# Performance work log

Measured on AMD Instinct MI355X. Metric: run time of the kernel, lower is better.

Reference implementation:

```python
import jax, jax.numpy as jnp
import numpy as np

LUMINANCE_Q = np.array([
    [16, 11, 10, 16, 24, 40, 51, 61],
    [12, 12, 14, 19, 26, 58, 60, 55],
    [14, 13, 16, 24, 40, 57, 69, 56],
    [14, 17, 22, 29, 51, 87, 80, 62],
    [18, 22, 37, 56, 68, 109, 103, 77],
    [24, 36, 55, 64, 81, 104, 113, 92],
    [49, 64, 78, 87, 103, 121, 120, 101],
    [72, 92, 95, 98, 112, 100, 103, 99]], dtype=np.float64) / 100.0

def _dct_matrix():
    # C[k, n] = grid_factors[k] * cos(pi*k*(2n+1)/16); grid_factors = 2*[1/sqrt(32), 1/sqrt(16)x7]
    k = np.arange(8)[:, None]
    n = np.arange(8)[None, :]
    a = np.full(8, 2.0 / np.sqrt(2 * 8))
    a[0] = 2.0 / np.sqrt(4 * 8)
    C = a[:, None] * np.cos(np.pi * k * (2 * n + 1) / 16.0)
    return jnp.asarray(C, dtype=jnp.float32)

DCT_C = _dct_matrix()
Q_TABLE = jnp.asarray(LUMINANCE_Q, dtype=jnp.float32)

def setup_inputs() -> dict:
    key = jax.random.key(0)
    k1, k2 = jax.random.split(key)
    B, H, W = 16, 1024, 1024
    # pixel-like values around 128
    image = 128.0 + 40.0 * jax.random.normal(k1, (B, 1, H, W), dtype=jnp.float32)
    quality_factor = jax.random.randint(k2, (B,), 1, 100).astype(jnp.float32)
    return {"image": image, "quality_factor": quality_factor}

def reference(image, quality_factor):
    B, _, H, W = image.shape
    # Set_QF: factor per batch element, shape [B,1,1,1,1]
    factor = jnp.where(quality_factor < 50.0,
                       5000.0 / quality_factor,
                       200.0 - 2.0 * quality_factor).reshape(B, 1, 1, 1, 1)
    # Image_2_Blocks: [B, H/8, 8, W/8, 8] -> [B, 8, 8, H/8, W/8], then center
    blocks = image.reshape(B, H // 8, 8, W // 8, 8).transpose(0, 2, 4, 1, 3) - 128.0
    # 2D orthonormal DCT-II over the two 8-wide in-block axes (axes 1 then 2)
    dct = jnp.einsum('un,vm,bnmij->buvij', DCT_C, DCT_C, blocks)
    out = dct / (factor * Q_TABLE[None, :, :, None, None])
    # quantize=False: no rounding
    return out.reshape(B, 64, H // 8, W // 8)
```

## Files before the change

kernel.cpp:

```cpp
#include <hip/hip_runtime.h>
#include <cstddef>


static constexpr float COSTAB[32] = {
     0.50000000000000000f,  0.49039264020161522f,  0.46193976625564337f,
     0.41573480615127262f,  0.35355339059327373f,  0.27778511650980114f,
     0.19134171618254492f,  0.09754516100806417f,  0.00000000000000000f,
    -0.09754516100806417f, -0.19134171618254492f, -0.27778511650980114f,
    -0.35355339059327373f, -0.41573480615127262f, -0.46193976625564337f,
    -0.49039264020161522f, -0.50000000000000000f, -0.49039264020161522f,
    -0.46193976625564337f, -0.41573480615127262f, -0.35355339059327373f,
    -0.27778511650980114f, -0.19134171618254492f, -0.09754516100806417f,
     0.00000000000000000f,  0.09754516100806417f,  0.19134171618254492f,
     0.27778511650980114f,  0.35355339059327373f,  0.41573480615127262f,
     0.46193976625564337f,  0.49039264020161522f,
};

__device__ __host__ __forceinline__ constexpr float dctC(int k, int n) {
    return (k == 0) ? 0.35355339059327373f
                    : COSTAB[(k * (2 * n + 1)) & 31];
}

static constexpr float LUMQ[64] = {
    16, 11, 10, 16, 24, 40, 51, 61,
    12, 12, 14, 19, 26, 58, 60, 55,
    14, 13, 16, 24, 40, 57, 69, 56,
    14, 17, 22, 29, 51, 87, 80, 62,
    18, 22, 37, 56, 68, 109, 103, 77,
    24, 36, 55, 64, 81, 104, 113, 92,
    49, 64, 78, 87, 103, 121, 120, 101,
    72, 92, 95, 98, 112, 100, 103, 99,
};

__device__ __host__ __forceinline__ constexpr float invQ(int u, int v) {
    return 100.0f / LUMQ[u * 8 + v];
}

__global__ __launch_bounds__(256) void jpeg_dct_quant_kernel(
    const float* __restrict__ img,
    const float* __restrict__ qfv,
    float* __restrict__ out)
{
    const int bid = blockIdx.x * 256 + threadIdx.x;
    const int j = bid & 127;
    const int i = (bid >> 7) & 127;
    const int b = bid >> 14;

    const float* src = img + ((size_t)b << 20) + (size_t)(i * 8) * 1024 + j * 8;

    float D[8][8];
    #pragma unroll
    for (int u = 0; u < 8; ++u)
        #pragma unroll
        for (int v = 0; v < 8; ++v)
            D[u][v] = 0.0f;

    #pragma unroll
    for (int n = 0; n < 8; ++n) {
        const float4 r0 = *reinterpret_cast<const float4*>(src + (size_t)n * 1024);
        const float4 r1 = *reinterpret_cast<const float4*>(src + (size_t)n * 1024 + 4);
        const float x[8] = {
            r0.x - 128.0f, r0.y - 128.0f, r0.z - 128.0f, r0.w - 128.0f,
            r1.x - 128.0f, r1.y - 128.0f, r1.z - 128.0f, r1.w - 128.0f,
        };

        float y[8];
        #pragma unroll
        for (int v = 0; v < 8; ++v) {
            float acc = 0.0f;
            #pragma unroll
            for (int m = 0; m < 8; ++m)
                acc += x[m] * dctC(v, m);
            y[v] = acc;
        }

        #pragma unroll
        for (int u = 0; u < 8; ++u) {
            const float cu = dctC(u, n);
            #pragma unroll
            for (int v = 0; v < 8; ++v)
                D[u][v] += cu * y[v];
        }
    }

    const float qf = qfv[b];
    const float factor = (qf < 50.0f) ? (5000.0f / qf) : (200.0f - 2.0f * qf);
    const float invf = 1.0f / factor;

    float* dst = out + ((size_t)b << 20) + (size_t)i * 128 + j;
    #pragma unroll
    for (int u = 0; u < 8; ++u)
        #pragma unroll
        for (int v = 0; v < 8; ++v)
            dst[(size_t)(u * 8 + v) * 16384] = D[u][v] * (invf * invQ(u, v));
}

extern "C" void kernel_launch(void* const* d_in, const int* in_sizes, int n_in,
                              void* d_out, int out_size, void* d_ws, size_t ws_size,
                              hipStream_t stream) {
    const float* img = (const float*)d_in[0];
    const float* qfv = (const float*)d_in[1];
    float* out = (float*)d_out;

    jpeg_dct_quant_kernel<<<1024, 256, 0, stream>>>(img, qfv, out);
}
```

Measured before the change: 111.3 us.

## Split DCT output rows across two threads, use even/odd butterfly, nontemporal stores

Each 8x8 block is now handled by two threads that each compute four of the eight output frequency rows, doubling the grid to 2048 blocks and halving the accumulator registers per thread. The row DCT uses an even/odd butterfly to halve multiplies, and the -128 centering is folded into a single DC correction of -1024. Output writes become nontemporal stores, and launch bounds request higher occupancy. The cost is that both threads of a pair load and transform the same input rows, so the row-pass work is duplicated.

```diff
diff --git a/kernel.cpp b/kernel.cpp
--- a/kernel.cpp
+++ b/kernel.cpp
@@ -36,52 +36,57 @@
     return 100.0f / LUMQ[u * 8 + v];
 }
 
-__global__ __launch_bounds__(256) void jpeg_dct_quant_kernel(
+__global__ __launch_bounds__(256, 6) void jpeg_dct_quant_kernel(
     const float* __restrict__ img,
     const float* __restrict__ qfv,
     float* __restrict__ out)
 {
-    const int bid = blockIdx.x * 256 + threadIdx.x;
-    const int j = bid & 127;
-    const int i = (bid >> 7) & 127;
-    const int b = bid >> 14;
+    const int tid  = threadIdx.x;
+    const int half = tid >> 7;
+    const int j    = tid & 127;
+    const int row  = blockIdx.x;
+    const int b    = row >> 7;
+    const int i    = row & 127;
+    const int u0   = half * 4;
 
     const float* src = img + ((size_t)b << 20) + (size_t)(i * 8) * 1024 + j * 8;
 
-    float D[8][8];
+    float acc[4][8];
     #pragma unroll
-    for (int u = 0; u < 8; ++u)
+    for (int uu = 0; uu < 4; ++uu)
         #pragma unroll
         for (int v = 0; v < 8; ++v)
-            D[u][v] = 0.0f;
+            acc[uu][v] = 0.0f;
 
     #pragma unroll
     for (int n = 0; n < 8; ++n) {
         const float4 r0 = *reinterpret_cast<const float4*>(src + (size_t)n * 1024);
         const float4 r1 = *reinterpret_cast<const float4*>(src + (size_t)n * 1024 + 4);
-        const float x[8] = {
-            r0.x - 128.0f, r0.y - 128.0f, r0.z - 128.0f, r0.w - 128.0f,
-            r1.x - 128.0f, r1.y - 128.0f, r1.z - 128.0f, r1.w - 128.0f,
-        };
+        const float s0 = r0.x + r1.w, s1 = r0.y + r1.z;
+        const float s2 = r0.z + r1.y, s3 = r0.w + r1.x;
+        const float d0 = r0.x - r1.w, d1 = r0.y - r1.z;
+        const float d2 = r0.z - r1.y, d3 = r0.w - r1.x;
 
         float y[8];
         #pragma unroll
-        for (int v = 0; v < 8; ++v) {
-            float acc = 0.0f;
-            #pragma unroll
-            for (int m = 0; m < 8; ++m)
-                acc += x[m] * dctC(v, m);
-            y[v] = acc;
-        }
+        for (int v = 0; v < 8; v += 2)
+            y[v] = s0 * dctC(v, 0) + s1 * dctC(v, 1)
+                 + s2 * dctC(v, 2) + s3 * dctC(v, 3);
+        #pragma unroll
+        for (int v = 1; v < 8; v += 2)
+            y[v] = d0 * dctC(v, 0) + d1 * dctC(v, 1)
+                 + d2 * dctC(v, 2) + d3 * dctC(v, 3);
 
         #pragma unroll
-        for (int u = 0; u < 8; ++u) {
-            const float cu = dctC(u, n);
+        for (int uu = 0; uu < 4; ++uu) {
+            const float cu = dctC(u0 + uu, n);
             #pragma unroll
             for (int v = 0; v < 8; ++v)
-                D[u][v] += cu * y[v];
+                acc[uu][v] += cu * y[v];
         }
     }
+
+    if (half == 0) acc[0][0] -= 1024.0f;
 
     const float qf = qfv[b];
     const float factor = (qf < 50.0f) ? (5000.0f / qf) : (200.0f - 2.0f * qf);
@@ -89,10 +94,14 @@
 
     float* dst = out + ((size_t)b << 20) + (size_t)i * 128 + j;
     #pragma unroll
-    for (int u = 0; u < 8; ++u)
+    for (int uu = 0; uu < 4; ++uu) {
+        const int u = u0 + uu;
         #pragma unroll
-        for (int v = 0; v < 8; ++v)
-            dst[(size_t)(u * 8 + v) * 16384] = D[u][v] * (invf * invQ(u, v));
+        for (int v = 0; v < 8; ++v) {
+            const float val = acc[uu][v] * (invf * invQ(u, v));
+            __builtin_nontemporal_store(val, dst + (size_t)(u * 8 + v) * 16384);
+        }
+    }
 }
 
 extern "C" void kernel_launch(void* const* d_in, const int* in_sizes, int n_in,
@@ -102,5 +111,5 @@
     const float* qfv = (const float*)d_in[1];
     float* out = (float*)d_out;
 
-    jpeg_dct_quant_kernel<<<1024, 256, 0, stream>>>(img, qfv, out);
+    jpeg_dct_quant_kernel<<<2048, 256, 0, stream>>>(img, qfv, out);
 }
```

Measured after the change: 186.5 us. +67.6%, slower.

## Replace matrix-multiply DCT with AAN fast butterfly DCT and folded scaling

Applied to the files above, without the earlier changes.

Replaces the dense separable 8x8 DCT matrix products with the Arai-Agui-Nakajima butterfly factorization applied to rows and then columns. The AAN output scale factors are folded into the per-coefficient quantization multiplier. The 128 centering is dropped from every pixel and applied once as a DC correction. This cuts per-block floating-point work substantially, but the kernel is likely bound by memory traffic, and the DC-offset trick changes rounding slightly.

```diff
diff --git a/kernel.cpp b/kernel.cpp
--- a/kernel.cpp
+++ b/kernel.cpp
@@ -2,26 +2,7 @@
 #include <cstddef>
 
 
-static constexpr float COSTAB[32] = {
-     0.50000000000000000f,  0.49039264020161522f,  0.46193976625564337f,
-     0.41573480615127262f,  0.35355339059327373f,  0.27778511650980114f,
-     0.19134171618254492f,  0.09754516100806417f,  0.00000000000000000f,
-    -0.09754516100806417f, -0.19134171618254492f, -0.27778511650980114f,
-    -0.35355339059327373f, -0.41573480615127262f, -0.46193976625564337f,
-    -0.49039264020161522f, -0.50000000000000000f, -0.49039264020161522f,
-    -0.46193976625564337f, -0.41573480615127262f, -0.35355339059327373f,
-    -0.27778511650980114f, -0.19134171618254492f, -0.09754516100806417f,
-     0.00000000000000000f,  0.09754516100806417f,  0.19134171618254492f,
-     0.27778511650980114f,  0.35355339059327373f,  0.41573480615127262f,
-     0.46193976625564337f,  0.49039264020161522f,
-};
-
-__device__ __host__ __forceinline__ constexpr float dctC(int k, int n) {
-    return (k == 0) ? 0.35355339059327373f
-                    : COSTAB[(k * (2 * n + 1)) & 31];
-}
-
-static constexpr float LUMQ[64] = {
+static constexpr double LUMQ[64] = {
     16, 11, 10, 16, 24, 40, 51, 61,
     12, 12, 14, 19, 26, 58, 60, 55,
     14, 13, 16, 24, 40, 57, 69, 56,
@@ -32,8 +13,46 @@
     72, 92, 95, 98, 112, 100, 103, 99,
 };
 
-__device__ __host__ __forceinline__ constexpr float invQ(int u, int v) {
-    return 100.0f / LUMQ[u * 8 + v];
+static constexpr double AANS[8] = {
+    1.0, 1.3870398453221475, 1.3065629648763766, 1.1758756024193588,
+    1.0, 0.7856949583871022, 0.5411961001461970, 0.2758993792829430,
+};
+
+__device__ __host__ __forceinline__ constexpr float outScale(int u, int v) {
+    return (float)(100.0 / (LUMQ[u * 8 + v] * 8.0 * AANS[u] * AANS[v]));
+}
+
+__device__ __forceinline__ void aan_dct8(float& x0, float& x1, float& x2,
+                                         float& x3, float& x4, float& x5,
+                                         float& x6, float& x7) {
+    const float t0 = x0 + x7, t7 = x0 - x7;
+    const float t1 = x1 + x6, t6 = x1 - x6;
+    const float t2 = x2 + x5, t5 = x2 - x5;
+    const float t3 = x3 + x4, t4 = x3 - x4;
+
+    float t10 = t0 + t3;
+    const float t13 = t0 - t3;
+    const float t11 = t1 + t2;
+    const float t12 = t1 - t2;
+    x0 = t10 + t11;
+    x4 = t10 - t11;
+    const float z1 = (t12 + t13) * 0.70710678118654752f;
+    x2 = t13 + z1;
+    x6 = t13 - z1;
+
+    t10 = t4 + t5;
+    const float u11 = t5 + t6;
+    const float u12 = t6 + t7;
+    const float z5 = (t10 - u12) * 0.38268343236508977f;
+    const float z2 = 0.54119610014619698f * t10 + z5;
+    const float z4 = 1.30656296487637653f * u12 + z5;
+    const float z3 = u11 * 0.70710678118654752f;
+    const float z11 = t7 + z3;
+    const float z13 = t7 - z3;
+    x5 = z13 + z2;
+    x3 = z13 - z2;
+    x1 = z11 + z4;
+    x7 = z11 - z4;
 }
 
 __global__ __launch_bounds__(256) void jpeg_dct_quant_kernel(
@@ -48,40 +67,26 @@
 
     const float* src = img + ((size_t)b << 20) + (size_t)(i * 8) * 1024 + j * 8;
 
-    float D[8][8];
-    #pragma unroll
-    for (int u = 0; u < 8; ++u)
-        #pragma unroll
-        for (int v = 0; v < 8; ++v)
-            D[u][v] = 0.0f;
-
+    float m[8][8];
     #pragma unroll
     for (int n = 0; n < 8; ++n) {
         const float4 r0 = *reinterpret_cast<const float4*>(src + (size_t)n * 1024);
         const float4 r1 = *reinterpret_cast<const float4*>(src + (size_t)n * 1024 + 4);
-        const float x[8] = {
-            r0.x - 128.0f, r0.y - 128.0f, r0.z - 128.0f, r0.w - 128.0f,
-            r1.x - 128.0f, r1.y - 128.0f, r1.z - 128.0f, r1.w - 128.0f,
-        };
+        m[n][0] = r0.x; m[n][1] = r0.y; m[n][2] = r0.z; m[n][3] = r0.w;
+        m[n][4] = r1.x; m[n][5] = r1.y; m[n][6] = r1.z; m[n][7] = r1.w;
+    }
 
-        float y[8];
-        #pragma unroll
-        for (int v = 0; v < 8; ++v) {
-            float acc = 0.0f;
-            #pragma unroll
-            for (int m = 0; m < 8; ++m)
-                acc += x[m] * dctC(v, m);
-            y[v] = acc;
-        }
+    #pragma unroll
+    for (int n = 0; n < 8; ++n)
+        aan_dct8(m[n][0], m[n][1], m[n][2], m[n][3],
+                 m[n][4], m[n][5], m[n][6], m[n][7]);
 
-        #pragma unroll
-        for (int u = 0; u < 8; ++u) {
-            const float cu = dctC(u, n);
-            #pragma unroll
-            for (int v = 0; v < 8; ++v)
-                D[u][v] += cu * y[v];
-        }
-    }
+    #pragma unroll
+    for (int v = 0; v < 8; ++v)
+        aan_dct8(m[0][v], m[1][v], m[2][v], m[3][v],
+                 m[4][v], m[5][v], m[6][v], m[7][v]);
+
+    m[0][0] -= 8192.0f;
 
     const float qf = qfv[b];
     const float factor = (qf < 50.0f) ? (5000.0f / qf) : (200.0f - 2.0f * qf);
@@ -92,7 +97,7 @@
     for (int u = 0; u < 8; ++u)
         #pragma unroll
         for (int v = 0; v < 8; ++v)
-            dst[(size_t)(u * 8 + v) * 16384] = D[u][v] * (invf * invQ(u, v));
+            dst[(size_t)(u * 8 + v) * 16384] = m[u][v] * (invf * outScale(u, v));
 }
 
 extern "C" void kernel_launch(void* const* d_in, const int* in_sizes, int n_in,
```

After: 111.5 us (median of 2 runs). About the same (+0.2%).
